# Performance work log

Measured on AMD Instinct MI355X. Metric: run time of the kernel, lower is better.

The kernel has to match this reference:

```python
import jax, jax.numpy as jnp
import numpy as np

N, D, IN, OUT, K = 50000, 16, 256, 128, 4  # nodes, sampled degree, input_size, output_size, heads
LEAKY_SLOPE = 0.01  # torch F.leaky_relu default


def setup_inputs() -> dict:
    key = jax.random.key(0)
    k1, k2, k3, k4 = jax.random.split(key, 4)
    X = jax.random.normal(k1, (N, IN), dtype=jnp.float32)
    W = jax.random.normal(k2, (K, OUT, IN), dtype=jnp.float32) * 0.05
    a = jax.random.normal(k3, (K, 2 * OUT), dtype=jnp.float32) * 0.05
    neighbor_idx = jax.random.randint(k4, (N, D), 0, N)  # fixed-degree neighbor sample
    return {"X": X, "W": W, "a": a, "neighbor_idx": neighbor_idx}


def reference(X, W, a, neighbor_idx):
    # X: [N, IN]; W: [K, OUT, IN]; a: [K, 2*OUT]; neighbor_idx: [N, D]
    out_dim = W.shape[1]
    # Per-head linear map of every node once: Wh[k, n] = W[k] @ X[n]
    Wh = jnp.einsum('koi,ni->kno', W, X)                       # [K, N, OUT]
    # a splits: first OUT weights multiply mapped neighbour, second OUT multiply mapped self
    a_nb, a_self = a[:, :out_dim], a[:, out_dim:]
    e_nb = jnp.einsum('kno,ko->kn', Wh, a_nb)                  # [K, N] score contribution as a neighbour
    e_self = jnp.einsum('kno,ko->kn', Wh, a_self)              # [K, N] score contribution as center node
    # Edge logits: e[k, i, d] = leaky_relu(a_nb.Wh[j] + a_self.Wh[i]), j = neighbor_idx[i, d]
    e = jax.nn.leaky_relu(e_nb[:, neighbor_idx] + e_self[:, :, None], LEAKY_SLOPE)  # [K, N, D]
    alpha = jax.nn.softmax(e, axis=-1)                         # softmax over each node's neighbour set
    Wh_nb = jnp.take(Wh, neighbor_idx, axis=1)                 # [K, N, D, OUT] gathered neighbour features
    h = jnp.einsum('knd,kndo->kno', alpha, Wh_nb)              # [K, N, OUT] attention-weighted aggregate
    # Concatenate heads along feature dim, matching per-node head-concat in the torch loop
    return jnp.transpose(h, (1, 0, 2)).reshape(X.shape[0], -1)  # [N, K*OUT]
```

## Files before the change

### kernel.cpp

```cpp
#include <hip/hip_runtime.h>

#define N_NODES 50000
#define D_NB 16
#define IN_DIM 256
#define OUT_DIM 128
#define K_HEADS 4
#define SLOPE 0.01f
#define NSLICE 16
#define SLICE_COLS 32

typedef __attribute__((ext_vector_type(8))) short short8;
typedef __attribute__((ext_vector_type(4))) float f32x4;

static __device__ __forceinline__ unsigned f2bf(float f) {
    unsigned u = __float_as_uint(f);
    unsigned r = u + 0x7fffu + ((u >> 16) & 1u);
    return r >> 16;
}
static __device__ __forceinline__ float bf2f(unsigned short b) {
    return __uint_as_float(((unsigned)b) << 16);
}

__global__ __launch_bounds__(256) void wb_kernel(
    const float* __restrict__ W, unsigned short* __restrict__ Wb)
{
    const int id = blockIdx.x * 256 + threadIdx.x;
    Wb[id] = (unsigned short)f2bf(W[id]);
}

__global__ __launch_bounds__(256) void wt8_kernel(
    const float* __restrict__ W, const float* __restrict__ a, float* __restrict__ wt8)
{
    const int v = blockIdx.x;
    const int k = v >> 1, s = v & 1;
    const int i = threadIdx.x;
    const float* av = a + k * 2 * OUT_DIM + s * OUT_DIM;
    float acc = 0.f;
    #pragma unroll 4
    for (int o = 0; o < OUT_DIM; ++o)
        acc += W[((size_t)k * OUT_DIM + o) * IN_DIM + i] * av[o];
    wt8[v * IN_DIM + i] = acc;
}

__global__ __launch_bounds__(256) void prep_kernel(
    const float* __restrict__ X, const float* __restrict__ wt8,
    unsigned short* __restrict__ Xb, float* __restrict__ e_nb4, float* __restrict__ e_self4)
{
    const int t = threadIdx.x;
    const int w = t >> 6;
    const int lane = t & 63;
    const int n = blockIdx.x * 4 + w;

    const f32x4 x = __builtin_nontemporal_load(
        (const f32x4*)(X + (size_t)n * IN_DIM + lane * 4));
    uint2 pk;
    pk.x = f2bf(x[0]) | (f2bf(x[1]) << 16);
    pk.y = f2bf(x[2]) | (f2bf(x[3]) << 16);
    *(uint2*)(Xb + (size_t)n * IN_DIM + lane * 4) = pk;

    float p[8];
    #pragma unroll
    for (int v = 0; v < 8; ++v) {
        const float4 wv = *(const float4*)(wt8 + v * IN_DIM + lane * 4);
        p[v] = x[0] * wv.x + x[1] * wv.y + x[2] * wv.z + x[3] * wv.w;
    }
    #pragma unroll
    for (int sh = 32; sh >= 1; sh >>= 1) {
        #pragma unroll
        for (int v = 0; v < 8; ++v) p[v] += __shfl_xor(p[v], sh);
    }
    if (lane == 0) {
        *(float4*)(e_nb4 + (size_t)n * 4)   = float4{p[0], p[2], p[4], p[6]};
        *(float4*)(e_self4 + (size_t)n * 4) = float4{p[1], p[3], p[5], p[7]};
    }
}

__global__ __launch_bounds__(256) void agg_kernel(
    const int* __restrict__ nidx, const unsigned short* __restrict__ Xb,
    const float* __restrict__ e_nb4, const float* __restrict__ e_self4,
    unsigned short* __restrict__ aggX, int n0, int nc)
{
    const int t = threadIdx.x;
    const int w = t >> 6;
    const int lane = t & 63;
    const int n = n0 + blockIdx.x * 4 + w;
    if (n >= n0 + nc || n >= N_NODES) return;

    const int k = lane >> 4;
    const int dl = lane & 15;

    const int nbr = __builtin_nontemporal_load(nidx + (size_t)n * D_NB + dl);
    const float4 eb4 = *(const float4*)(e_nb4 + (size_t)nbr * 4);
    const float4 es4 = *(const float4*)(e_self4 + (size_t)n * 4);
    const float en = (k & 2) ? ((k & 1) ? eb4.w : eb4.z) : ((k & 1) ? eb4.y : eb4.x);
    const float es = (k & 2) ? ((k & 1) ? es4.w : es4.z) : ((k & 1) ? es4.y : es4.x);
    const float x = en + es;
    const float v = x > 0.f ? x : SLOPE * x;
    float m = v;
    #pragma unroll
    for (int sh = 8; sh >= 1; sh >>= 1) m = fmaxf(m, __shfl_xor(m, sh, 16));
    const float pz = __expf(v - m);
    float sum = pz;
    #pragma unroll
    for (int sh = 8; sh >= 1; sh >>= 1) sum += __shfl_xor(sum, sh, 16);
    const float alpha = pz / sum;

    float acc[4][4] = {};
    #pragma unroll
    for (int h = 0; h < 2; ++h) {
        uint2 u[8];
        #pragma unroll
        for (int b = 0; b < 8; ++b) {
            const int nd = __shfl(nbr, h * 8 + b);
            u[b] = *(const uint2*)(Xb + (size_t)nd * IN_DIM + lane * 4);
        }
        #pragma unroll
        for (int b = 0; b < 8; ++b) {
            const float x0 = bf2f((unsigned short)(u[b].x & 0xffffu));
            const float x1 = bf2f((unsigned short)(u[b].x >> 16));
            const float x2 = bf2f((unsigned short)(u[b].y & 0xffffu));
            const float x3 = bf2f((unsigned short)(u[b].y >> 16));
            #pragma unroll
            for (int kk = 0; kk < 4; ++kk) {
                const float ad = __shfl(alpha, kk * 16 + h * 8 + b);
                acc[kk][0] += ad * x0;
                acc[kk][1] += ad * x1;
                acc[kk][2] += ad * x2;
                acc[kk][3] += ad * x3;
            }
        }
    }
    #pragma unroll
    for (int kk = 0; kk < 4; ++kk) {
        uint2 pk;
        pk.x = f2bf(acc[kk][0]) | (f2bf(acc[kk][1]) << 16);
        pk.y = f2bf(acc[kk][2]) | (f2bf(acc[kk][3]) << 16);
        *(uint2*)(aggX + ((size_t)kk * nc + (n - n0)) * IN_DIM + lane * 4) = pk;
    }
}

__global__ __launch_bounds__(512) void gemm2_kernel(
    const unsigned short* __restrict__ aggX, const unsigned short* __restrict__ Wb,
    float* __restrict__ out, int n0, int nc)
{
    __shared__ unsigned short Wlds[2][SLICE_COLS * IN_DIM];

    const int t = threadIdx.x;
    const int lane = t & 63;
    const int w = t >> 6;
    const int lrow = lane & 15;
    const int lk = lane >> 4;
    const int m0 = n0 + blockIdx.x * 128 + w * 16;

    const int arow = m0 + lrow;
    const bool avalid = (arow < n0 + nc) && (arow < N_NODES);

    auto STAGE = [&](int st, int buf) {
        const unsigned short* WbS = Wb + (size_t)st * SLICE_COLS * IN_DIM;
        #pragma unroll
        for (int i = 0; i < 2; ++i) {
            const int c = i * 512 + t;
            const int r = c >> 5;
            const int p = c & 31;
            const int cu = p ^ (r & 7);
            const unsigned short* gsrc = WbS + r * IN_DIM + cu * 8;
            unsigned short* ldst = &Wlds[buf][c * 8];
            __builtin_amdgcn_global_load_lds(
                (const __attribute__((address_space(1))) void*)gsrc,
                (__attribute__((address_space(3))) void*)ldst, 16, 0, 0);
        }
    };

    short8 af[2][8];
    auto LOADAF = [&](int head, int slot) {
        const unsigned short* Ar = aggX + ((size_t)head * nc + (arow - n0)) * IN_DIM + lk * 8;
        #pragma unroll
        for (int kk = 0; kk < 8; ++kk)
            af[slot][kk] = avalid ? *(const short8*)(Ar + kk * 32)
                                  : short8{0, 0, 0, 0, 0, 0, 0, 0};
    };

    STAGE(0, 0);
    LOADAF(0, 0);
    __syncthreads();

    #pragma unroll
    for (int st = 0; st < NSLICE; ++st) {
        const int buf = st & 1;
        if (st + 1 < NSLICE) STAGE(st + 1, buf ^ 1);
        if ((st & 3) == 3 && st + 1 < NSLICE)
            LOADAF((st >> 2) + 1, ((st >> 2) + 1) & 1);

        const int slot = (st >> 2) & 1;
        f32x4 acc[2] = {};
        #pragma unroll
        for (int kk = 0; kk < 8; ++kk) {
            #pragma unroll
            for (int nt = 0; nt < 2; ++nt) {
                const int row = nt * 16 + lrow;
                const int pos = (kk * 4 + lk) ^ (row & 7);
                const short8 bf = *(const short8*)(&Wlds[buf][row * IN_DIM + pos * 8]);
                acc[nt] = __builtin_amdgcn_mfma_f32_16x16x32_bf16(bf, af[slot][kk], acc[nt], 0, 0, 0);
            }
        }

        const int k = st >> 2, cb = st & 3;
        if (avalid) {
            const size_t cbase = (size_t)arow * (K_HEADS * OUT_DIM)
                               + (size_t)k * OUT_DIM + cb * SLICE_COLS + lk * 4;
            #pragma unroll
            for (int nt = 0; nt < 2; ++nt)
                *(f32x4*)(out + cbase + nt * 16) = acc[nt];
        }
        __syncthreads();
    }
}

extern "C" void kernel_launch(void* const* d_in, const int* in_sizes, int n_in,
                              void* d_out, int out_size, void* d_ws, size_t ws_size,
                              hipStream_t stream) {
    const float* X = (const float*)d_in[0];
    const float* W = (const float*)d_in[1];
    const float* a = (const float*)d_in[2];
    const int* nidx = (const int*)d_in[3];
    float* out = (float*)d_out;

    const size_t WbB  = (size_t)K_HEADS * OUT_DIM * IN_DIM * 2;
    const size_t XbB  = (size_t)N_NODES * IN_DIM * 2;
    const size_t wt8B = (size_t)8 * IN_DIM * 4;
    const size_t eB   = (size_t)K_HEADS * N_NODES * 4;
    auto need = [&](int nc) {
        return WbB + XbB + wt8B + 2 * eB + (size_t)K_HEADS * nc * IN_DIM * 2 + 1024;
    };

    int np, nc;
    if      (ws_size >= need(50000)) { np = 1; nc = 50000; }
    else if (ws_size >= need(25000)) { np = 2; nc = 25000; }
    else                             { np = 4; nc = 12500; }

    char* p = (char*)d_ws;
    unsigned short* Wb   = (unsigned short*)p;   p += WbB;
    unsigned short* Xb   = (unsigned short*)p;   p += XbB;
    float*          wt8  = (float*)p;            p += wt8B;
    float*          enb4 = (float*)p;            p += eB;
    float*          esf4 = (float*)p;            p += eB;
    unsigned short* aggX = (unsigned short*)p;

    hipLaunchKernelGGL(wb_kernel, dim3(2048), dim3(256), 0, stream, W, Wb);
    hipLaunchKernelGGL(wt8_kernel, dim3(8), dim3(256), 0, stream, W, a, wt8);

    hipLaunchKernelGGL(prep_kernel,
        dim3(N_NODES / 4), dim3(256), 0, stream, X, wt8, Xb, enb4, esf4);

    for (int pass = 0; pass < np; ++pass) {
        const int nb0 = pass * nc;
        hipLaunchKernelGGL(agg_kernel,
            dim3((nc + 3) / 4), dim3(256), 0, stream, nidx, Xb, enb4, esf4, aggX, nb0, nc);
        hipLaunchKernelGGL(gemm2_kernel,
            dim3((nc + 127) / 128), dim3(512), 0, stream, aggX, Wb, out, nb0, nc);
    }
}
```

Baseline: 160.1 us.

## Fuse weight prep kernels and split neighbor gathers across wave halves with 16B loads

Merges the bf16 weight conversion and attention-vector projection into a single launch, removing one kernel launch. In the aggregation kernel, each half-wave now gathers a different neighbor's row with 16-byte loads (8 bf16 per lane), so all 8 loads are issued up front instead of two batches of 8-byte loads. Partial sums from the two halves are combined with a cross-half shuffle and only half the lanes store. This adds 32 shuffle-adds per node and doubles per-lane accumulators, which raises register pressure.

```diff
diff --git a/kernel.cpp b/kernel.cpp
--- a/kernel.cpp
+++ b/kernel.cpp
@@ -21,17 +21,16 @@
     return __uint_as_float(((unsigned)b) << 16);
 }
 
-__global__ __launch_bounds__(256) void wb_kernel(
-    const float* __restrict__ W, unsigned short* __restrict__ Wb)
-{
-    const int id = blockIdx.x * 256 + threadIdx.x;
-    Wb[id] = (unsigned short)f2bf(W[id]);
-}
-
-__global__ __launch_bounds__(256) void wt8_kernel(
-    const float* __restrict__ W, const float* __restrict__ a, float* __restrict__ wt8)
-{
-    const int v = blockIdx.x;
+__global__ __launch_bounds__(256) void prep_w_kernel(
+    const float* __restrict__ W, const float* __restrict__ a,
+    unsigned short* __restrict__ Wb, float* __restrict__ wt8)
+{
+    if (blockIdx.x < 2048) {
+        const int id = blockIdx.x * 256 + threadIdx.x;
+        Wb[id] = (unsigned short)f2bf(W[id]);
+        return;
+    }
+    const int v = blockIdx.x - 2048;
     const int k = v >> 1, s = v & 1;
     const int i = threadIdx.x;
     const float* av = a + k * 2 * OUT_DIM + s * OUT_DIM;
@@ -88,14 +87,16 @@
 
     const int k = lane >> 4;
     const int dl = lane & 15;
+    const int hi = lane >> 5;
+    const int cq = lane & 31;
 
     const int nbr = __builtin_nontemporal_load(nidx + (size_t)n * D_NB + dl);
     const float4 eb4 = *(const float4*)(e_nb4 + (size_t)nbr * 4);
     const float4 es4 = *(const float4*)(e_self4 + (size_t)n * 4);
     const float en = (k & 2) ? ((k & 1) ? eb4.w : eb4.z) : ((k & 1) ? eb4.y : eb4.x);
     const float es = (k & 2) ? ((k & 1) ? es4.w : es4.z) : ((k & 1) ? es4.y : es4.x);
-    const float x = en + es;
-    const float v = x > 0.f ? x : SLOPE * x;
+    const float xv = en + es;
+    const float v = xv > 0.f ? xv : SLOPE * xv;
     float m = v;
     #pragma unroll
     for (int sh = 8; sh >= 1; sh >>= 1) m = fmaxf(m, __shfl_xor(m, sh, 16));
@@ -105,37 +106,48 @@
     for (int sh = 8; sh >= 1; sh >>= 1) sum += __shfl_xor(sum, sh, 16);
     const float alpha = pz / sum;
 
-    float acc[4][4] = {};
-    #pragma unroll
-    for (int h = 0; h < 2; ++h) {
-        uint2 u[8];
-        #pragma unroll
-        for (int b = 0; b < 8; ++b) {
-            const int nd = __shfl(nbr, h * 8 + b);
-            u[b] = *(const uint2*)(Xb + (size_t)nd * IN_DIM + lane * 4);
-        }
-        #pragma unroll
-        for (int b = 0; b < 8; ++b) {
-            const float x0 = bf2f((unsigned short)(u[b].x & 0xffffu));
-            const float x1 = bf2f((unsigned short)(u[b].x >> 16));
-            const float x2 = bf2f((unsigned short)(u[b].y & 0xffffu));
-            const float x3 = bf2f((unsigned short)(u[b].y >> 16));
+    uint4 u[8];
+    #pragma unroll
+    for (int b = 0; b < 8; ++b) {
+        const int nd = __shfl(nbr, 2 * b + hi);
+        u[b] = *(const uint4*)(Xb + (size_t)nd * IN_DIM + cq * 8);
+    }
+
+    float acc[4][8] = {};
+    #pragma unroll
+    for (int b = 0; b < 8; ++b) {
+        float xe[8];
+        xe[0] = bf2f((unsigned short)(u[b].x & 0xffffu));
+        xe[1] = bf2f((unsigned short)(u[b].x >> 16));
+        xe[2] = bf2f((unsigned short)(u[b].y & 0xffffu));
+        xe[3] = bf2f((unsigned short)(u[b].y >> 16));
+        xe[4] = bf2f((unsigned short)(u[b].z & 0xffffu));
+        xe[5] = bf2f((unsigned short)(u[b].z >> 16));
+        xe[6] = bf2f((unsigned short)(u[b].w & 0xffffu));
+        xe[7] = bf2f((unsigned short)(u[b].w >> 16));
+        #pragma unroll
+        for (int kk = 0; kk < 4; ++kk) {
+            const float ad = __shfl(alpha, kk * 16 + 2 * b + hi);
             #pragma unroll
-            for (int kk = 0; kk < 4; ++kk) {
-                const float ad = __shfl(alpha, kk * 16 + h * 8 + b);
-                acc[kk][0] += ad * x0;
-                acc[kk][1] += ad * x1;
-                acc[kk][2] += ad * x2;
-                acc[kk][3] += ad * x3;
-            }
-        }
-    }
-    #pragma unroll
-    for (int kk = 0; kk < 4; ++kk) {
-        uint2 pk;
-        pk.x = f2bf(acc[kk][0]) | (f2bf(acc[kk][1]) << 16);
-        pk.y = f2bf(acc[kk][2]) | (f2bf(acc[kk][3]) << 16);
-        *(uint2*)(aggX + ((size_t)kk * nc + (n - n0)) * IN_DIM + lane * 4) = pk;
+            for (int c = 0; c < 8; ++c) acc[kk][c] += ad * xe[c];
+        }
+    }
+    #pragma unroll
+    for (int kk = 0; kk < 4; ++kk)
+        #pragma unroll
+        for (int c = 0; c < 8; ++c)
+            acc[kk][c] += __shfl_xor(acc[kk][c], 32);
+
+    if (hi == 0) {
+        #pragma unroll
+        for (int kk = 0; kk < 4; ++kk) {
+            uint4 pk;
+            pk.x = f2bf(acc[kk][0]) | (f2bf(acc[kk][1]) << 16);
+            pk.y = f2bf(acc[kk][2]) | (f2bf(acc[kk][3]) << 16);
+            pk.z = f2bf(acc[kk][4]) | (f2bf(acc[kk][5]) << 16);
+            pk.w = f2bf(acc[kk][6]) | (f2bf(acc[kk][7]) << 16);
+            *(uint4*)(aggX + ((size_t)kk * nc + (n - n0)) * IN_DIM + cq * 8) = pk;
+        }
     }
 }
 
@@ -246,8 +258,7 @@
     float*          esf4 = (float*)p;            p += eB;
     unsigned short* aggX = (unsigned short*)p;
 
-    hipLaunchKernelGGL(wb_kernel, dim3(2048), dim3(256), 0, stream, W, Wb);
-    hipLaunchKernelGGL(wt8_kernel, dim3(8), dim3(256), 0, stream, W, a, wt8);
+    hipLaunchKernelGGL(prep_w_kernel, dim3(2056), dim3(256), 0, stream, W, a, Wb, wt8);
 
     hipLaunchKernelGGL(prep_kernel,
         dim3(N_NODES / 4), dim3(256), 0, stream, X, wt8, Xb, enb4, esf4);
```

Result: no change. 159.2 us (-0.6%).

## Merge weight prep kernels and double rows per block in output GEMM

Applied to the files above, without the earlier changes.

Folds the W-to-bf16 conversion and the attention-vector projection into one launch, removing a kernel launch. The output GEMM now gives each wave two 16-row tiles, 256 rows per block, so every W slice staged in LDS feeds twice as many MFMAs and W is re-read from global memory half as often. The A-fragment prefetch is no longer double-buffered and the slice loop is no longer fully unrolled. Register pressure also rises, which may cut occupancy and weaken latency hiding.

```diff
diff --git a/kernel.cpp b/kernel.cpp
--- a/kernel.cpp
+++ b/kernel.cpp
@@ -21,17 +21,16 @@
     return __uint_as_float(((unsigned)b) << 16);
 }
 
-__global__ __launch_bounds__(256) void wb_kernel(
-    const float* __restrict__ W, unsigned short* __restrict__ Wb)
-{
-    const int id = blockIdx.x * 256 + threadIdx.x;
-    Wb[id] = (unsigned short)f2bf(W[id]);
-}
-
-__global__ __launch_bounds__(256) void wt8_kernel(
-    const float* __restrict__ W, const float* __restrict__ a, float* __restrict__ wt8)
-{
-    const int v = blockIdx.x;
+__global__ __launch_bounds__(256) void prep_w_kernel(
+    const float* __restrict__ W, const float* __restrict__ a,
+    unsigned short* __restrict__ Wb, float* __restrict__ wt8)
+{
+    if (blockIdx.x < 2048) {
+        const int id = blockIdx.x * 256 + threadIdx.x;
+        Wb[id] = (unsigned short)f2bf(W[id]);
+        return;
+    }
+    const int v = blockIdx.x - 2048;
     const int k = v >> 1, s = v & 1;
     const int i = threadIdx.x;
     const float* av = a + k * 2 * OUT_DIM + s * OUT_DIM;
@@ -94,8 +93,8 @@
     const float4 es4 = *(const float4*)(e_self4 + (size_t)n * 4);
     const float en = (k & 2) ? ((k & 1) ? eb4.w : eb4.z) : ((k & 1) ? eb4.y : eb4.x);
     const float es = (k & 2) ? ((k & 1) ? es4.w : es4.z) : ((k & 1) ? es4.y : es4.x);
-    const float x = en + es;
-    const float v = x > 0.f ? x : SLOPE * x;
+    const float xv = en + es;
+    const float v = xv > 0.f ? xv : SLOPE * xv;
     float m = v;
     #pragma unroll
     for (int sh = 8; sh >= 1; sh >>= 1) m = fmaxf(m, __shfl_xor(m, sh, 16));
@@ -150,10 +149,12 @@
     const int w = t >> 6;
     const int lrow = lane & 15;
     const int lk = lane >> 4;
-    const int m0 = n0 + blockIdx.x * 128 + w * 16;
-
-    const int arow = m0 + lrow;
-    const bool avalid = (arow < n0 + nc) && (arow < N_NODES);
+    const int m0 = n0 + blockIdx.x * 256 + w * 16;
+
+    const int arow0 = m0 + lrow;
+    const int arow1 = arow0 + 128;
+    const bool av0 = (arow0 < n0 + nc) && (arow0 < N_NODES);
+    const bool av1 = (arow1 < n0 + nc) && (arow1 < N_NODES);
 
     auto STAGE = [&](int st, int buf) {
         const unsigned short* WbS = Wb + (size_t)st * SLICE_COLS * IN_DIM;
@@ -171,28 +172,28 @@
         }
     };
 
-    short8 af[2][8];
-    auto LOADAF = [&](int head, int slot) {
-        const unsigned short* Ar = aggX + ((size_t)head * nc + (arow - n0)) * IN_DIM + lk * 8;
-        #pragma unroll
-        for (int kk = 0; kk < 8; ++kk)
-            af[slot][kk] = avalid ? *(const short8*)(Ar + kk * 32)
-                                  : short8{0, 0, 0, 0, 0, 0, 0, 0};
+    short8 af0[8], af1[8];
+    auto LOADAF = [&](int head) {
+        const size_t hb = (size_t)head * nc;
+        const unsigned short* Ar0 = aggX + (hb + (arow0 - n0)) * IN_DIM + lk * 8;
+        const unsigned short* Ar1 = aggX + (hb + (arow1 - n0)) * IN_DIM + lk * 8;
+        #pragma unroll
+        for (int kk = 0; kk < 8; ++kk) {
+            af0[kk] = av0 ? *(const short8*)(Ar0 + kk * 32) : short8{0,0,0,0,0,0,0,0};
+            af1[kk] = av1 ? *(const short8*)(Ar1 + kk * 32) : short8{0,0,0,0,0,0,0,0};
+        }
     };
 
     STAGE(0, 0);
-    LOADAF(0, 0);
+    LOADAF(0);
     __syncthreads();
 
-    #pragma unroll
     for (int st = 0; st < NSLICE; ++st) {
         const int buf = st & 1;
         if (st + 1 < NSLICE) STAGE(st + 1, buf ^ 1);
-        if ((st & 3) == 3 && st + 1 < NSLICE)
-            LOADAF((st >> 2) + 1, ((st >> 2) + 1) & 1);
-
-        const int slot = (st >> 2) & 1;
-        f32x4 acc[2] = {};
+        if ((st & 3) == 0 && st) LOADAF(st >> 2);
+
+        f32x4 acc0[2] = {}, acc1[2] = {};
         #pragma unroll
         for (int kk = 0; kk < 8; ++kk) {
             #pragma unroll
@@ -200,17 +201,17 @@
                 const int row = nt * 16 + lrow;
                 const int pos = (kk * 4 + lk) ^ (row & 7);
                 const short8 bf = *(const short8*)(&Wlds[buf][row * IN_DIM + pos * 8]);
-                acc[nt] = __builtin_amdgcn_mfma_f32_16x16x32_bf16(bf, af[slot][kk], acc[nt], 0, 0, 0);
+                acc0[nt] = __builtin_amdgcn_mfma_f32_16x16x32_bf16(bf, af0[kk], acc0[nt], 0, 0, 0);
+                acc1[nt] = __builtin_amdgcn_mfma_f32_16x16x32_bf16(bf, af1[kk], acc1[nt], 0, 0, 0);
             }
         }
 
         const int k = st >> 2, cb = st & 3;
-        if (avalid) {
-            const size_t cbase = (size_t)arow * (K_HEADS * OUT_DIM)
-                               + (size_t)k * OUT_DIM + cb * SLICE_COLS + lk * 4;
-            #pragma unroll
-            for (int nt = 0; nt < 2; ++nt)
-                *(f32x4*)(out + cbase + nt * 16) = acc[nt];
+        const size_t cbase = (size_t)k * OUT_DIM + cb * SLICE_COLS + lk * 4;
+        #pragma unroll
+        for (int nt = 0; nt < 2; ++nt) {
+            if (av0) *(f32x4*)(out + (size_t)arow0 * (K_HEADS * OUT_DIM) + cbase + nt * 16) = acc0[nt];
+            if (av1) *(f32x4*)(out + (size_t)arow1 * (K_HEADS * OUT_DIM) + cbase + nt * 16) = acc1[nt];
         }
         __syncthreads();
     }
@@ -246,8 +247,7 @@
     float*          esf4 = (float*)p;            p += eB;
     unsigned short* aggX = (unsigned short*)p;
 
-    hipLaunchKernelGGL(wb_kernel, dim3(2048), dim3(256), 0, stream, W, Wb);
-    hipLaunchKernelGGL(wt8_kernel, dim3(8), dim3(256), 0, stream, W, a, wt8);
+    hipLaunchKernelGGL(prep_w_kernel, dim3(2056), dim3(256), 0, stream, W, a, Wb, wt8);
 
     hipLaunchKernelGGL(prep_kernel,
         dim3(N_NODES / 4), dim3(256), 0, stream, X, wt8, Xb, enb4, esf4);
@@ -257,6 +257,6 @@
         hipLaunchKernelGGL(agg_kernel,
             dim3((nc + 3) / 4), dim3(256), 0, stream, nidx, Xb, enb4, esf4, aggX, nb0, nc);
         hipLaunchKernelGGL(gemm2_kernel,
-            dim3((nc + 127) / 128), dim3(512), 0, stream, aggX, Wb, out, nb0, nc);
-    }
-}
+            dim3((nc + 255) / 256), dim3(512), 0, stream, aggX, Wb, out, nb0, nc);
+    }
+}
```

Measured after the change: 159.9 us. Within noise of the previous version (-0.1%).
